# Kernel tuning notes

Measured on AMD Instinct MI355X. Metric: run time of the kernel, lower is better.

Reference implementation:

```python
import jax, jax.numpy as jnp
import numpy as np

B, L, U, H = 32, 2048, 512, 8
HD = U // H  # head_dim = 64


def _conv1d(x, w, b, pad):
    # x: (B, Cin, L), w: (Cout, Cin, K) -> (B, Cout, L)
    y = jax.lax.conv_general_dilated(
        x, w, window_strides=(1,), padding=[(pad, pad)],
        dimension_numbers=("NCH", "OIH", "NCH"))
    return y + b[None, :, None]


def _maxpool1d_k3(x):
    # kernel=3, stride=1, pad=1, same as nn.MaxPool1d(3,1,1)
    return jax.lax.reduce_window(
        x, -jnp.inf, jax.lax.max,
        window_dimensions=(1, 1, 3), window_strides=(1, 1, 1),
        padding=[(0, 0), (0, 0), (1, 1)])


def setup_inputs() -> dict:
    key = jax.random.key(0)
    ks = jax.random.split(key, 12)
    s = 0.02
    return {
        "t": jax.random.normal(ks[0], (B, L, U), jnp.float32),
        "g": jax.random.normal(ks[1], (B, 1, U), jnp.float32),
        "g_mask": jnp.ones((B, 1), jnp.int32),
        "t_mask": jax.random.randint(ks[2], (B, L), 0, 2).astype(jnp.int32),
        "Wq": jax.random.normal(ks[3], (U, U, 3), jnp.float32) * s,
        "bq": jnp.zeros((U,), jnp.float32),
        "Wk": jax.random.normal(ks[4], (U, U, 3), jnp.float32) * s,
        "bk": jnp.zeros((U,), jnp.float32),
        "Wv": jax.random.normal(ks[5], (U, U, 3), jnp.float32) * s,
        "bv": jnp.zeros((U,), jnp.float32),
        "Wh": jax.random.normal(ks[6], (H, H, 1), jnp.float32) * s,
        "bh": jnp.zeros((H,), jnp.float32),
        "Wo": jax.random.normal(ks[7], (U, U, 1), jnp.float32) * s,
        "bo": jnp.zeros((U,), jnp.float32),
    }


def reference(t, g, g_mask, t_mask, Wq, bq, Wk, bk, Wv, bv, Wh, bh, Wo, bo):
    x = t.transpose(0, 2, 1)                      # (B, U, L)
    q = _conv1d(x, Wq, bq, 1)                     # (B, U, L)
    k = _conv1d(x, Wk, bk, 1)
    v = _conv1d(x, Wv, bv, 1)

    # global query: max over sequence -> (B, H, 1, HD)
    q_ = q.max(-1).reshape(B, H, 1, HD)
    # keys: [global max key, maxpooled local keys] -> (B, H, 1+L, HD)
    k_g = k.max(-1).reshape(B, H, 1, HD)
    k_c = _maxpool1d_k3(k).reshape(B, H, HD, L).transpose(0, 1, 3, 2)
    key_ = jnp.concatenate([k_g, k_c], axis=2)
    v_g = v.max(-1).reshape(B, H, 1, HD)
    v_c = _maxpool1d_k3(v).reshape(B, H, HD, L).transpose(0, 1, 3, 2)
    value_ = jnp.concatenate([v_g, v_c], axis=2)

    attn = jnp.einsum("bhqd,bhkd->bhqk", q_, key_) / jnp.sqrt(jnp.float32(U))
    key_mask = jnp.concatenate([g_mask, t_mask], axis=-1)  # (B, 1+L)
    attn = jnp.where(key_mask[:, None, None, :] == 0, -jnp.inf, attn)
    attn = jax.nn.softmax(attn, axis=-1)
    # query mask multiply (g_mask broadcast over heads & keys)
    attn = attn * g_mask[:, None, :, None].astype(jnp.float32)

    out = jnp.einsum("bhqk,bhkd->bhqd", attn, value_)  # (B, H, 1, HD)
    out = out.reshape(B, H, HD)
    # conv1d_h: 1x1 conv mixing heads
    out = jnp.einsum("oi,bid->bod", Wh[:, :, 0], out) + bh[None, :, None]
    out = out.reshape(B, H, 1, HD).transpose(0, 2, 1, 3).reshape(B, 1, U)
    # conv1d_out: 1x1 conv over channels
    out = jnp.einsum("oi,bqi->bqo", Wo[:, :, 0], out) + bo
    return out  # (B, 1, U)
```

## Files before the change

kernel.cpp:

```cpp
#include <hip/hip_runtime.h>
#include <hip/hip_fp16.h>

#define B_  32
#define L_  2048
#define U_  512
#define H_  8
#define HD_ 64

typedef __attribute__((ext_vector_type(8))) _Float16 half8;
typedef __attribute__((ext_vector_type(4))) float f32x4;

__device__ __forceinline__ unsigned fmap(float x) {
    unsigned u = __float_as_uint(x);
    return (u & 0x80000000u) ? ~u : (u | 0x80000000u);
}
__device__ __forceinline__ float funmap(unsigned m) {
    unsigned bits = (m & 0x80000000u) ? (m ^ 0x80000000u) : ~m;
    return __uint_as_float(bits);
}

__global__ void __launch_bounds__(256) t_cvt(const float* __restrict__ t,
                                             __half* __restrict__ t16) {
    const size_t id = (size_t)blockIdx.x * 256 + threadIdx.x;
    const float4 a = *(const float4*)(t + id * 8);
    const float4 b = *(const float4*)(t + id * 8 + 4);
    auto p0 = __builtin_amdgcn_cvt_pkrtz(a.x, a.y);
    auto p1 = __builtin_amdgcn_cvt_pkrtz(a.z, a.w);
    auto p2 = __builtin_amdgcn_cvt_pkrtz(b.x, b.y);
    auto p3 = __builtin_amdgcn_cvt_pkrtz(b.z, b.w);
    half8 hv;
    hv[0] = p0[0]; hv[1] = p0[1]; hv[2] = p1[0]; hv[3] = p1[1];
    hv[4] = p2[0]; hv[5] = p2[1]; hv[6] = p3[0]; hv[7] = p3[1];
    *(half8*)(t16 + id * 8) = hv;
}

__global__ void repack_w2(const float* __restrict__ Wq,
                          const float* __restrict__ Wk,
                          const float* __restrict__ Wv,
                          __half* __restrict__ Wrp2) {
    int id = blockIdx.x * 256 + threadIdx.x;
    int mb2  = id / 12288;
    int rem  = id % 12288;
    int F    = rem >> 6;
    int lane = rem & 63;
    int mblk = mb2 >> 1, wm = mb2 & 1;
    int mi = F & 3, ks = (F >> 2) & 1, t3 = F >> 3;
    int kk = t3 % 3, iblk = t3 / 3;
    int mat = mblk >> 2;
    const float* W = (mat == 0) ? Wq : (mat == 1) ? Wk : Wv;
    int ol = ((mblk & 3) << 7) + wm * 64 + mi * 16 + (lane & 15);
    int ib = iblk * 64 + ks * 32 + (lane >> 4) * 8;
    half8 hv;
#pragma unroll
    for (int j = 0; j < 8; ++j)
        hv[j] = (_Float16)W[(ol * 512 + ib + j) * 3 + kk];
    *(half8*)(Wrp2 + (size_t)id * 8) = hv;
}

__global__ void wot_repack(const float* __restrict__ Wo, float* __restrict__ WoT) {
    int id = blockIdx.x * 256 + threadIdx.x;
    int o = id & 511, i = id >> 9;
    WoT[(size_t)i * 512 + o] = Wo[(size_t)o * 512 + i];
}

__global__ void __launch_bounds__(256, 3) conv_gemm(
    const __half* __restrict__ t16,
    const __half* __restrict__ Wrp2,
    const float* __restrict__ bq,
    const float* __restrict__ bk,
    const float* __restrict__ bv,
    __half* __restrict__ kbuf, __half* __restrict__ vbuf,
    unsigned* __restrict__ qmaxU, unsigned* __restrict__ kmaxU,
    unsigned* __restrict__ vmaxU) {
    __shared__ __align__(16) __half lB16[2][130 * 64];

    const int tid  = threadIdx.x;
    const int lane = tid & 63;
    const int w    = tid >> 6;
    const int wm = w >> 1, wn = w & 1;
    const int xcd  = blockIdx.x & 7;
    const int slot = blockIdx.x >> 3;
    const int ntile = xcd + 8 * (slot / 12);
    const int mblk  = slot % 12;
    const int bb = ntile >> 4;
    const int l0 = (ntile & 15) << 7;
    const int lane15 = lane & 15, kgrp = lane >> 4;

    const char* Abase = (const char*)Wrp2 + (size_t)(mblk * 2 + wm) * 196608;
    const __half* tB = t16 + (size_t)bb * L_ * U_;

    f32x4 acc[4][4];
#pragma unroll
    for (int a = 0; a < 4; ++a)
#pragma unroll
        for (int c = 0; c < 4; ++c) acc[a][c] = (f32x4){0.f, 0.f, 0.f, 0.f};

    auto stageB = [&](int nb, int buf) {
        const int i0 = nb << 6;
#pragma unroll
        for (int d = 0; d < 4; ++d) {
            const int rowb = w * 32 + d * 8;
            const int row  = rowb + (lane >> 3);
            const int l    = l0 - 1 + row;
            const int p8   = lane & 7;
            const char* g = (const char*)(tB + (size_t)l * U_ + i0) + ((p8 ^ (l & 7)) << 4);
            if (l >= 0 && l < L_)
                __builtin_amdgcn_global_load_lds(
                    (const __attribute__((address_space(1))) unsigned int*)g,
                    (__attribute__((address_space(3))) unsigned int*)((char*)lB16[buf] + rowb * 128),
                    16, 0, 0);
        }
        if (w == 0 && lane < 16) {
            const int row = 128 + (lane >> 3);
            const int l   = l0 - 1 + row;
            const int p8  = lane & 7;
            const char* g = (const char*)(tB + (size_t)l * U_ + i0) + ((p8 ^ (l & 7)) << 4);
            if (l >= 0 && l < L_)
                __builtin_amdgcn_global_load_lds(
                    (const __attribute__((address_space(1))) unsigned int*)g,
                    (__attribute__((address_space(3))) unsigned int*)((char*)lB16[buf] + 128 * 128),
                    16, 0, 0);
        }
    };

    if (l0 == 0 && tid < 64) {
        lB16[0][tid] = (__half)0.f; lB16[1][tid] = (__half)0.f;
    }
    if (l0 == 1920 && tid < 64) {
        lB16[0][129 * 64 + tid] = (__half)0.f; lB16[1][129 * 64 + tid] = (__half)0.f;
    }

    stageB(0, 0);
    __syncthreads();

    for (int iblk = 0; iblk < 8; ++iblk) {
        const int cur = iblk & 1;
        const char* bbase = (const char*)lB16[cur];
#pragma unroll
        for (int kk = 0; kk < 3; ++kk) {
#pragma unroll
            for (int ks = 0; ks < 2; ++ks) {
                half8 af[4];
#pragma unroll
                for (int mi = 0; mi < 4; ++mi)
                    af[mi] = *(const half8*)(Abase +
                        ((((size_t)iblk * 3 + kk) * 2 + ks) * 4 + mi) * 1024 + lane * 16);
                if (kk == 0 && ks == 0 && iblk < 7) stageB(iblk + 1, cur ^ 1);
                half8 bfr[4];
#pragma unroll
                for (int ni = 0; ni < 4; ++ni) {
                    const int rbuf = wn * 64 + ni * 16 + lane15 + kk;
                    const int key  = (rbuf + 7) & 7;
                    const int p    = ks * 4 + kgrp;
                    bfr[ni] = *(const half8*)(bbase + rbuf * 128 + ((p ^ key) << 4));
                }
#pragma unroll
                for (int mi = 0; mi < 4; ++mi)
#pragma unroll
                    for (int ni = 0; ni < 4; ++ni)
                        acc[mi][ni] = __builtin_amdgcn_mfma_f32_16x16x32_f16(
                            af[mi], bfr[ni], acc[mi][ni], 0, 0, 0);
            }
        }
        __syncthreads();
    }

    const int mat = mblk >> 2;
    const float* bias = (mat == 0) ? bq : (mat == 1) ? bk : bv;
    const int oBase = ((mblk & 3) << 7) + wm * 64 + kgrp * 4;
#pragma unroll
    for (int mi = 0; mi < 4; ++mi) {
#pragma unroll
        for (int r = 0; r < 4; ++r) {
            const int o = oBase + mi * 16 + r;
            const float bsv = bias[o];
            float vals[4];
            float mx = -3.0e38f;
#pragma unroll
            for (int ni = 0; ni < 4; ++ni) {
                float v = acc[mi][ni][r] + bsv;
                vals[ni] = v;
                mx = fmaxf(mx, v);
            }
#pragma unroll
            for (int d = 1; d < 16; d <<= 1) mx = fmaxf(mx, __shfl_xor(mx, d, 64));
            if (mat == 0) {
                if (lane15 == 0) atomicMax(&qmaxU[bb * U_ + o], fmap(mx));
            } else {
                __half* buf = (mat == 1) ? kbuf : vbuf;
                size_t rowbase = ((size_t)bb * U_ + o) * L_ + l0 + wn * 64;
#pragma unroll
                for (int ni = 0; ni < 4; ++ni)
                    buf[rowbase + ni * 16 + lane15] = __float2half(vals[ni]);
                unsigned* mptr = (mat == 1) ? kmaxU : vmaxU;
                if (lane15 == 0) atomicMax(&mptr[bb * U_ + o], fmap(mx));
            }
        }
    }
}

__global__ void __launch_bounds__(1024) attn_kernel(
    const __half* __restrict__ kbuf, const __half* __restrict__ vbuf,
    const unsigned* __restrict__ qmaxU, const unsigned* __restrict__ kmaxU,
    const unsigned* __restrict__ vmaxU,
    const int* __restrict__ g_mask, const int* __restrict__ t_mask,
    float* __restrict__ attout) {
    const int bh = blockIdx.x;
    const int b = bh >> 3, h = bh & 7;
    const int tid = threadIdx.x;
    const int lane = tid & 63;
    __shared__ float qs[64], kg[64], vg[64];
    __shared__ float pl[2048];
    __shared__ float red[1024];
    if (tid < 64) {
        qs[tid] = funmap(qmaxU[b * U_ + h * 64 + tid]);
        kg[tid] = funmap(kmaxU[b * U_ + h * 64 + tid]);
        vg[tid] = funmap(vmaxU[b * U_ + h * 64 + tid]);
    }
    __syncthreads();
    const float scale = 0.044194173824159216f;

    const __half* kbase = kbuf + ((size_t)b * U_ + h * 64) * L_;
    const int l0 = tid * 2;
    float acc0 = 0.f, acc1 = 0.f;
    for (int o = 0; o < 64; ++o) {
        const __half* row = kbase + (size_t)o * L_;
        const __half2 hv = *(const __half2*)(row + l0);
        float f1 = __half2float(hv.x), f2 = __half2float(hv.y);
        float fL = __shfl_up(f2, 1, 64);
        float fR = __shfl_down(f1, 1, 64);
        if (lane == 0)  fL = (l0 == 0) ? -3.0e38f : __half2float(row[l0 - 1]);
        if (lane == 63) fR = (l0 + 2 >= L_) ? -3.0e38f : __half2float(row[l0 + 2]);
        const float qw = qs[o];
        acc0 += qw * fmaxf(fL, fmaxf(f1, f2));
        acc1 += qw * fmaxf(f1, fmaxf(f2, fR));
    }
    float lmax = -3.0e38f;
    {
        int tm0 = t_mask[b * L_ + l0], tm1 = t_mask[b * L_ + l0 + 1];
        float lg0 = (tm0 == 0) ? -INFINITY : acc0 * scale;
        float lg1 = (tm1 == 0) ? -INFINITY : acc1 * scale;
        pl[l0] = lg0; pl[l0 + 1] = lg1;
        lmax = fmaxf(lg0, lg1);
    }
    float ag = 0.f;
    for (int d = 0; d < 64; ++d) ag += qs[d] * kg[d];
    const int gm = g_mask[b];
    float lgg = gm ? ag * scale : -INFINITY;
    red[tid] = lmax; __syncthreads();
    for (int s = 512; s > 0; s >>= 1) {
        if (tid < s) red[tid] = fmaxf(red[tid], red[tid + s]);
        __syncthreads();
    }
    float mx = fmaxf(red[0], lgg);
    __syncthreads();
    {
        float lg0 = pl[l0], lg1 = pl[l0 + 1];
        float e0 = (lg0 <= -3.0e38f) ? 0.f : __expf(lg0 - mx);
        float e1 = (lg1 <= -3.0e38f) ? 0.f : __expf(lg1 - mx);
        pl[l0] = e0; pl[l0 + 1] = e1;
        red[tid] = e0 + e1;
    }
    __syncthreads();
    for (int s = 512; s > 0; s >>= 1) {
        if (tid < s) red[tid] += red[tid + s];
        __syncthreads();
    }
    float eg = gm ? __expf(lgg - mx) : 0.f;
    float den = red[0] + eg;
    if (!(den > 0.f)) den = 1.f;
    __syncthreads();
    const int o = tid >> 4;
    const int ch = tid & 15;
    const __half* vrow = vbuf + ((size_t)b * U_ + h * 64 + o) * L_;
    float s = 0.f;
    for (int lb = ch * 128; lb < ch * 128 + 128; lb += 8) {
        union { uint4 u; __half hh[8]; } pk;
        pk.u = *(const uint4*)(vrow + lb);
        float f[10];
#pragma unroll
        for (int j = 0; j < 8; ++j) f[j + 1] = __half2float(pk.hh[j]);
        f[0] = (lb == 0) ? -3.0e38f : __half2float(vrow[lb - 1]);
        f[9] = (lb + 8 >= L_) ? -3.0e38f : __half2float(vrow[lb + 8]);
#pragma unroll
        for (int j = 0; j < 8; ++j)
            s += pl[lb + j] * fmaxf(f[j], fmaxf(f[j + 1], f[j + 2]));
    }
    red[tid] = s; __syncthreads();
    if (ch == 0) {
        float tot = 0.f;
#pragma unroll
        for (int q2 = 0; q2 < 16; ++q2) tot += red[(o << 4) + q2];
        float val = (eg * vg[o] + tot) / den;
        val *= (float)gm;
        attout[(size_t)b * U_ + h * 64 + o] = val;
    }
}

__global__ void __launch_bounds__(512) out_kernel(
    const float* __restrict__ attout,
    const float* __restrict__ Wh, const float* __restrict__ bh,
    const float* __restrict__ WoT, const float* __restrict__ bo,
    float* __restrict__ out) {
    const int b = blockIdx.x;
    const int tid = threadIdx.x;
    __shared__ float tmp[512];
    const int oh = tid >> 6, d = tid & 63;
    float s = bh[oh];
#pragma unroll
    for (int i = 0; i < 8; ++i)
        s += Wh[oh * 8 + i] * attout[b * U_ + i * 64 + d];
    tmp[oh * 64 + d] = s;
    __syncthreads();
    float s2 = bo[tid];
    for (int i = 0; i < 512; ++i) s2 += WoT[i * 512 + tid] * tmp[i];
    out[b * U_ + tid] = s2;
}

extern "C" void kernel_launch(void* const* d_in, const int* in_sizes, int n_in,
                              void* d_out, int out_size, void* d_ws, size_t ws_size,
                              hipStream_t stream) {
    const float* t  = (const float*)d_in[0];
    const int* g_mask = (const int*)d_in[2];
    const int* t_mask = (const int*)d_in[3];
    const float* Wq = (const float*)d_in[4];
    const float* bq = (const float*)d_in[5];
    const float* Wk = (const float*)d_in[6];
    const float* bk = (const float*)d_in[7];
    const float* Wv = (const float*)d_in[8];
    const float* bv = (const float*)d_in[9];
    const float* Wh = (const float*)d_in[10];
    const float* bh = (const float*)d_in[11];
    const float* Wo = (const float*)d_in[12];
    const float* bo = (const float*)d_in[13];

    char* ws = (char*)d_ws;
    __half* Wrp2 = (__half*)ws;
    float* WoT   = (float*)(ws + 4718592);
    __half* t16  = (__half*)(ws + 5767168);
    __half* kbuf = (__half*)(ws + 5767168 + 67108864);
    __half* vbuf = (__half*)(ws + 5767168 + 2 * 67108864);
    unsigned* qmaxU = (unsigned*)(ws + 5767168 + 3 * 67108864);
    unsigned* kmaxU = qmaxU + 16384;
    unsigned* vmaxU = kmaxU + 16384;
    float* attout = (float*)(vmaxU + 16384);

    (void)hipMemsetAsync(qmaxU, 0, 3 * 16384 * sizeof(unsigned), stream);
    t_cvt<<<16384, 256, 0, stream>>>(t, t16);
    repack_w2<<<1152, 256, 0, stream>>>(Wq, Wk, Wv, Wrp2);
    wot_repack<<<1024, 256, 0, stream>>>(Wo, WoT);
    conv_gemm<<<6144, 256, 0, stream>>>(t16, Wrp2, bq, bk, bv, kbuf, vbuf,
                                        qmaxU, kmaxU, vmaxU);
    attn_kernel<<<256, 1024, 0, stream>>>(kbuf, vbuf, qmaxU, kmaxU, vmaxU,
                                          g_mask, t_mask, attout);
    out_kernel<<<32, 512, 0, stream>>>(attout, Wh, bh, WoT, bo, (float*)d_out);
}
```

Before: 688.7 us.

## Load conv B operand directly from global memory, dropping LDS staging

Removes the double-buffered LDS staging of the input tile in the conv GEMM. Each wave now reads its B fragments straight from global memory (via L1/L2), with a templated edge path that clamps and zeroes the padded rows. Without LDS and barriers the occupancy hint goes from 3 to 4 blocks per CU. Separately, the attention-value loop is re-indexed so neighbouring threads read neighbouring 8-element chunks, which coalesces the loads. The main risk is redundant global/L1 traffic: the three kernel-tap shifts and the two M-waves re-read the same rows that the LDS tile used to share.

```diff
diff --git a/kernel.cpp b/kernel.cpp
--- a/kernel.cpp
+++ b/kernel.cpp
@@ -9,6 +9,8 @@
 
 typedef __attribute__((ext_vector_type(8))) _Float16 half8;
 typedef __attribute__((ext_vector_type(4))) float f32x4;
+
+template <bool V> struct BoolC { static constexpr bool value = V; };
 
 __device__ __forceinline__ unsigned fmap(float x) {
     unsigned u = __float_as_uint(x);
@@ -63,7 +65,7 @@
     WoT[(size_t)i * 512 + o] = Wo[(size_t)o * 512 + i];
 }
 
-__global__ void __launch_bounds__(256, 3) conv_gemm(
+__global__ void __launch_bounds__(256, 4) conv_gemm(
     const __half* __restrict__ t16,
     const __half* __restrict__ Wrp2,
     const float* __restrict__ bq,
@@ -72,8 +74,6 @@
     __half* __restrict__ kbuf, __half* __restrict__ vbuf,
     unsigned* __restrict__ qmaxU, unsigned* __restrict__ kmaxU,
     unsigned* __restrict__ vmaxU) {
-    __shared__ __align__(16) __half lB16[2][130 * 64];
-
     const int tid  = threadIdx.x;
     const int lane = tid & 63;
     const int w    = tid >> 6;
@@ -95,64 +95,34 @@
 #pragma unroll
         for (int c = 0; c < 4; ++c) acc[a][c] = (f32x4){0.f, 0.f, 0.f, 0.f};
 
-    auto stageB = [&](int nb, int buf) {
-        const int i0 = nb << 6;
-#pragma unroll
-        for (int d = 0; d < 4; ++d) {
-            const int rowb = w * 32 + d * 8;
-            const int row  = rowb + (lane >> 3);
-            const int l    = l0 - 1 + row;
-            const int p8   = lane & 7;
-            const char* g = (const char*)(tB + (size_t)l * U_ + i0) + ((p8 ^ (l & 7)) << 4);
-            if (l >= 0 && l < L_)
-                __builtin_amdgcn_global_load_lds(
-                    (const __attribute__((address_space(1))) unsigned int*)g,
-                    (__attribute__((address_space(3))) unsigned int*)((char*)lB16[buf] + rowb * 128),
-                    16, 0, 0);
-        }
-        if (w == 0 && lane < 16) {
-            const int row = 128 + (lane >> 3);
-            const int l   = l0 - 1 + row;
-            const int p8  = lane & 7;
-            const char* g = (const char*)(tB + (size_t)l * U_ + i0) + ((p8 ^ (l & 7)) << 4);
-            if (l >= 0 && l < L_)
-                __builtin_amdgcn_global_load_lds(
-                    (const __attribute__((address_space(1))) unsigned int*)g,
-                    (__attribute__((address_space(3))) unsigned int*)((char*)lB16[buf] + 128 * 128),
-                    16, 0, 0);
-        }
-    };
-
-    if (l0 == 0 && tid < 64) {
-        lB16[0][tid] = (__half)0.f; lB16[1][tid] = (__half)0.f;
-    }
-    if (l0 == 1920 && tid < 64) {
-        lB16[0][129 * 64 + tid] = (__half)0.f; lB16[1][129 * 64 + tid] = (__half)0.f;
-    }
-
-    stageB(0, 0);
-    __syncthreads();
-
-    for (int iblk = 0; iblk < 8; ++iblk) {
-        const int cur = iblk & 1;
-        const char* bbase = (const char*)lB16[cur];
-#pragma unroll
-        for (int kk = 0; kk < 3; ++kk) {
-#pragma unroll
-            for (int ks = 0; ks < 2; ++ks) {
+    const int base_l = l0 - 1 + wn * 64 + lane15;
+
+    auto mainloop = [&](auto EDGE_) {
+        constexpr bool EDGE = decltype(EDGE_)::value;
+        for (int iblk = 0; iblk < 8; ++iblk) {
+            const int i0 = iblk << 6;
+#pragma unroll
+            for (int s = 0; s < 6; ++s) {
+                const int kk = s >> 1, ks = s & 1;
                 half8 af[4];
 #pragma unroll
                 for (int mi = 0; mi < 4; ++mi)
                     af[mi] = *(const half8*)(Abase +
                         ((((size_t)iblk * 3 + kk) * 2 + ks) * 4 + mi) * 1024 + lane * 16);
-                if (kk == 0 && ks == 0 && iblk < 7) stageB(iblk + 1, cur ^ 1);
                 half8 bfr[4];
 #pragma unroll
                 for (int ni = 0; ni < 4; ++ni) {
-                    const int rbuf = wn * 64 + ni * 16 + lane15 + kk;
-                    const int key  = (rbuf + 7) & 7;
-                    const int p    = ks * 4 + kgrp;
-                    bfr[ni] = *(const half8*)(bbase + rbuf * 128 + ((p ^ key) << 4));
+                    int l = base_l + ni * 16 + kk;
+                    if (EDGE) {
+                        const bool ok = (unsigned)l < (unsigned)L_;
+                        int lcl = l < 0 ? 0 : (l > L_ - 1 ? L_ - 1 : l);
+                        half8 v = *(const half8*)(tB + (size_t)lcl * U_ +
+                                                  i0 + ks * 32 + kgrp * 8);
+                        bfr[ni] = ok ? v : half8{};
+                    } else {
+                        bfr[ni] = *(const half8*)(tB + (size_t)l * U_ +
+                                                  i0 + ks * 32 + kgrp * 8);
+                    }
                 }
 #pragma unroll
                 for (int mi = 0; mi < 4; ++mi)
@@ -162,8 +132,9 @@
                             af[mi], bfr[ni], acc[mi][ni], 0, 0, 0);
             }
         }
-        __syncthreads();
-    }
+    };
+    if (l0 == 0 || l0 == (L_ - 128)) mainloop(BoolC<true>{});
+    else                             mainloop(BoolC<false>{});
 
     const int mat = mblk >> 2;
     const float* bias = (mat == 0) ? bq : (mat == 1) ? bk : bv;
@@ -274,7 +245,8 @@
     const int ch = tid & 15;
     const __half* vrow = vbuf + ((size_t)b * U_ + h * 64 + o) * L_;
     float s = 0.f;
-    for (int lb = ch * 128; lb < ch * 128 + 128; lb += 8) {
+    for (int it = 0; it < 16; ++it) {
+        const int lb = it * 128 + ch * 8;
         union { uint4 u; __half hh[8]; } pk;
         pk.u = *(const uint4*)(vrow + lb);
         float f[10];
```

New measurement: 1.203 ms. 74.6% more time.
